# Optimization experiments

Measured on AMD Instinct MI355X. Metric: run time of the kernel, lower is better.

## Reference

```python
import jax, jax.numpy as jnp
import numpy as np

N_NODES = 100000

def _sage_conv(x, src, dst, Wl, bl, Wr, n_nodes):
    # PyG SAGEConv (mean aggr): out = lin_l(mean_{j in N(i)} x_j) + lin_r(x_i)
    msgs = x[src]                                            # [E, d] gather
    agg = jax.ops.segment_sum(msgs, dst, num_segments=n_nodes)   # [N, d]
    cnt = jax.ops.segment_sum(jnp.ones((src.shape[0],), x.dtype), dst,
                              num_segments=n_nodes)          # [N]
    mean = agg / jnp.maximum(cnt, 1.0)[:, None]              # mean aggregation
    return mean @ Wl.T + bl + x @ Wr.T

def setup_inputs() -> dict:
    key = jax.random.key(0)
    ks = jax.random.split(key, 6)
    d_in, d_hid, d_out = 64, 64, 2
    n_edges = 1600000
    x = jax.random.normal(ks[0], (N_NODES, d_in), dtype=jnp.float32)
    edge_index = jax.random.randint(ks[1], (2, n_edges), 0, N_NODES, dtype=jnp.int64)
    s = 1.0 / np.sqrt(d_in)
    W1l = jax.random.uniform(ks[2], (d_hid, d_in), jnp.float32, -s, s)
    b1l = jnp.zeros((d_hid,), jnp.float32)
    W1r = jax.random.uniform(ks[3], (d_hid, d_in), jnp.float32, -s, s)
    s2 = 1.0 / np.sqrt(d_hid)
    W2l = jax.random.uniform(ks[4], (d_out, d_hid), jnp.float32, -s2, s2)
    b2l = jnp.zeros((d_out,), jnp.float32)
    W2r = jax.random.uniform(ks[5], (d_out, d_hid), jnp.float32, -s2, s2)
    return {"x": x, "edge_index": edge_index, "W1l": W1l, "b1l": b1l,
            "W1r": W1r, "W2l": W2l, "b2l": b2l, "W2r": W2r}

def reference(x, edge_index, W1l, b1l, W1r, W2l, b2l, W2r):
    src, dst = edge_index[0], edge_index[1]
    h = _sage_conv(x, src, dst, W1l, b1l, W1r, N_NODES)
    h = jax.nn.relu(h)
    # F.dropout(p=0.5, training=False) is identity at inference
    out = _sage_conv(h, src, dst, W2l, b2l, W2r, N_NODES)
    return out
```

## Files before the change

kernel.cpp:

```cpp
#include <hip/hip_runtime.h>
#include <cstdint>

typedef long long i64;
typedef unsigned int u32;


#define BKT_SHIFT 8
#define BKT_MAX   512
#define BKT_CAP   5120
#define CHUNK     2048

__device__ __forceinline__ int edge_at(const void* eidx, int is64, size_t i) {
  return is64 ? (int)((const i64*)eidx)[i] : ((const int*)eidx)[i];
}

__global__ __launch_bounds__(256) void k_pre(const void* __restrict__ eidx,
                                             int* __restrict__ gcount, u32* __restrict__ pairs, int E,
                                             const float* __restrict__ x,
                                             const float* __restrict__ Wl, const float* __restrict__ bl,
                                             const float* __restrict__ Wr,
                                             float* __restrict__ XL, float* __restrict__ XR,
                                             int n_nodes, int nbkt) {
  __shared__ float smem[64 * 68 * 3];
  int tid = threadIdx.x;

  if ((int)blockIdx.x < nbkt) {
    int* hist   = (int*)smem;
    int* basech = hist + BKT_MAX;
    int* run    = basech + BKT_MAX;
    int* nzp    = run + BKT_MAX;
    for (int i = tid; i < BKT_MAX; i += 256) { hist[i] = 0; run[i] = 0; }
    if (tid == 0) *nzp = 0;
    __syncthreads();
    if (((const int*)eidx)[2 * tid + 1] != 0) *nzp = 1;
    __syncthreads();
    int is64 = (*nzp == 0);

    int cbase = blockIdx.x * CHUNK;
    int sreg[8], dreg[8];
#pragma unroll
    for (int i = 0; i < 8; ++i) {
      int e = cbase + tid + 256 * i;
      bool v = e < E;
      sreg[i] = v ? edge_at(eidx, is64, (size_t)e) : 0;
      dreg[i] = v ? edge_at(eidx, is64, (size_t)E + e) : -1;
      if (v) atomicAdd(&hist[dreg[i] >> BKT_SHIFT], 1);
    }
    __syncthreads();
    for (int i = tid; i < BKT_MAX; i += 256) {
      int h = hist[i];
      basech[i] = h ? (i * BKT_CAP + atomicAdd(&gcount[i], h)) : 0;
    }
    __syncthreads();
#pragma unroll
    for (int i = 0; i < 8; ++i) {
      if (dreg[i] >= 0) {
        int b = dreg[i] >> BKT_SHIFT;
        int r = atomicAdd(&run[b], 1);
        pairs[basech[b] + r] = ((u32)sreg[i] << 8) | (u32)(dreg[i] & 255);
      }
    }
    return;
  }

  float* sWl = smem;
  float* sWr = smem + 64 * 68;
  float* sX  = smem + 2 * 64 * 68;
  int base = (blockIdx.x - nbkt) * 64;

#pragma unroll
  for (int r = 0; r < 4; ++r) {
    int idx = tid + 256 * r;
    int f = idx >> 4, c4 = idx & 15;
    float4 wl = *(const float4*)(Wl + f * 64 + c4 * 4);
    float4 wr = *(const float4*)(Wr + f * 64 + c4 * 4);
    sWl[(c4 * 4 + 0) * 68 + f] = wl.x; sWl[(c4 * 4 + 1) * 68 + f] = wl.y;
    sWl[(c4 * 4 + 2) * 68 + f] = wl.z; sWl[(c4 * 4 + 3) * 68 + f] = wl.w;
    sWr[(c4 * 4 + 0) * 68 + f] = wr.x; sWr[(c4 * 4 + 1) * 68 + f] = wr.y;
    sWr[(c4 * 4 + 2) * 68 + f] = wr.z; sWr[(c4 * 4 + 3) * 68 + f] = wr.w;
  }
#pragma unroll
  for (int r = 0; r < 4; ++r) {
    int idx = tid + 256 * r;
    int nn = idx >> 4, c4 = idx & 15;
    int node = base + nn;
    float4 xv = make_float4(0.f, 0.f, 0.f, 0.f);
    if (node < n_nodes) xv = *(const float4*)(x + (size_t)node * 64 + c4 * 4);
    sX[(c4 * 4 + 0) * 68 + nn] = xv.x; sX[(c4 * 4 + 1) * 68 + nn] = xv.y;
    sX[(c4 * 4 + 2) * 68 + nn] = xv.z; sX[(c4 * 4 + 3) * 68 + nn] = xv.w;
  }
  __syncthreads();

  int f0 = (tid & 15) * 4, n0 = (tid >> 4) * 4;
  float accL[4][4] = {{0}}, accR[4][4] = {{0}};
#pragma unroll 8
  for (int k = 0; k < 64; ++k) {
    float4 xv = *(const float4*)&sX[k * 68 + n0];
    float4 wl = *(const float4*)&sWl[k * 68 + f0];
    float4 wr = *(const float4*)&sWr[k * 68 + f0];
    float xn[4] = {xv.x, xv.y, xv.z, xv.w};
    float wlf[4] = {wl.x, wl.y, wl.z, wl.w};
    float wrf[4] = {wr.x, wr.y, wr.z, wr.w};
#pragma unroll
    for (int a = 0; a < 4; ++a)
#pragma unroll
      for (int b = 0; b < 4; ++b) {
        accL[a][b] += xn[a] * wlf[b];
        accR[a][b] += xn[a] * wrf[b];
      }
  }

  float4 blv = *(const float4*)(bl + f0);
#pragma unroll
  for (int a = 0; a < 4; ++a) {
    int node = base + n0 + a;
    if (node >= n_nodes) continue;
    float4 ol = make_float4(accL[a][0], accL[a][1], accL[a][2], accL[a][3]);
    float4 orr = make_float4(accR[a][0] + blv.x, accR[a][1] + blv.y,
                             accR[a][2] + blv.z, accR[a][3] + blv.w);
    *(float4*)(XL + (size_t)node * 64 + f0) = ol;
    *(float4*)(XR + (size_t)node * 64 + f0) = orr;
  }
}

__global__ __launch_bounds__(512) void k_csr(const int* __restrict__ gcount, const u32* __restrict__ pairs,
                                             int* __restrict__ csr_src, int* __restrict__ rs,
                                             int* __restrict__ re, int n_nodes) {
  __shared__ int cnt[256];
  __shared__ int sc[256];
  __shared__ int cur[256];
  int b = blockIdx.x, t = threadIdx.x;
  if (t < 256) cnt[t] = 0;
  __syncthreads();
  int n = gcount[b];
  int lo = b * BKT_CAP, hi = lo + n;
  int tail = n & 3;
  for (int i = lo + t * 4; i + 3 < hi; i += 2048) {
    uint4 p = *(const uint4*)(pairs + i);
    atomicAdd(&cnt[p.x & 255], 1); atomicAdd(&cnt[p.y & 255], 1);
    atomicAdd(&cnt[p.z & 255], 1); atomicAdd(&cnt[p.w & 255], 1);
  }
  if (t < tail) atomicAdd(&cnt[pairs[hi - tail + t] & 255], 1);
  __syncthreads();
  int v = (t < 256) ? cnt[t] : 0;
  if (t < 256) sc[t] = v;
  __syncthreads();
  for (int off = 1; off < 256; off <<= 1) {
    int a = (t >= off && t < 256) ? sc[t - off] : 0;
    __syncthreads();
    if (t < 256) sc[t] += a;
    __syncthreads();
  }
  if (t < 256) {
    int start = lo + sc[t] - v;
    int node = (b << BKT_SHIFT) + t;
    if (node < n_nodes) { rs[node] = start; re[node] = start + v; }
    cur[t] = start;
  }
  __syncthreads();
  for (int i = lo + t * 4; i + 3 < hi; i += 2048) {
    uint4 p = *(const uint4*)(pairs + i);
    csr_src[atomicAdd(&cur[p.x & 255], 1)] = (int)(p.x >> 8);
    csr_src[atomicAdd(&cur[p.y & 255], 1)] = (int)(p.y >> 8);
    csr_src[atomicAdd(&cur[p.z & 255], 1)] = (int)(p.z >> 8);
    csr_src[atomicAdd(&cur[p.w & 255], 1)] = (int)(p.w >> 8);
  }
  if (t < tail) {
    u32 p = pairs[hi - tail + t];
    csr_src[atomicAdd(&cur[p & 255], 1)] = (int)(p >> 8);
  }
}

__global__ __launch_bounds__(256) void k_agg1g2(const int* __restrict__ rs, const int* __restrict__ re,
                                                const int* __restrict__ csr_src,
                                                const float* __restrict__ XL, const float* __restrict__ XR,
                                                const float* __restrict__ W2l, const float* __restrict__ b2l,
                                                const float* __restrict__ W2r,
                                                float* __restrict__ HL, float* __restrict__ HR,
                                                int n_nodes) {
  int wave = threadIdx.x >> 6, lane = threadIdx.x & 63;
  int g = lane >> 4, c = lane & 15;
  int n = (blockIdx.x * 4 + wave) * 4 + g;
  if (n >= n_nodes) return;

  float4 wl0 = *(const float4*)(W2l + c * 4);
  float4 wl1 = *(const float4*)(W2l + 64 + c * 4);
  float4 wr0 = *(const float4*)(W2r + c * 4);
  float4 wr1 = *(const float4*)(W2r + 64 + c * 4);
  float4 xr = *(const float4*)(XR + (size_t)n * 64 + c * 4);

  int start = rs[n], end = re[n];
  float4 a0 = make_float4(0.f, 0.f, 0.f, 0.f);
  float4 a1 = make_float4(0.f, 0.f, 0.f, 0.f);
  float4 a2 = make_float4(0.f, 0.f, 0.f, 0.f);
  float4 a3 = make_float4(0.f, 0.f, 0.f, 0.f);
  int e = start;
  for (; e + 7 < end; e += 8) {
    int s0 = csr_src[e],     s1 = csr_src[e + 1], s2 = csr_src[e + 2], s3 = csr_src[e + 3];
    int s4 = csr_src[e + 4], s5 = csr_src[e + 5], s6 = csr_src[e + 6], s7 = csr_src[e + 7];
    float4 v0 = *(const float4*)(XL + (size_t)s0 * 64 + c * 4);
    float4 v1 = *(const float4*)(XL + (size_t)s1 * 64 + c * 4);
    float4 v2 = *(const float4*)(XL + (size_t)s2 * 64 + c * 4);
    float4 v3 = *(const float4*)(XL + (size_t)s3 * 64 + c * 4);
    float4 v4 = *(const float4*)(XL + (size_t)s4 * 64 + c * 4);
    float4 v5 = *(const float4*)(XL + (size_t)s5 * 64 + c * 4);
    float4 v6 = *(const float4*)(XL + (size_t)s6 * 64 + c * 4);
    float4 v7 = *(const float4*)(XL + (size_t)s7 * 64 + c * 4);
    a0.x += v0.x; a0.y += v0.y; a0.z += v0.z; a0.w += v0.w;
    a1.x += v1.x; a1.y += v1.y; a1.z += v1.z; a1.w += v1.w;
    a2.x += v2.x; a2.y += v2.y; a2.z += v2.z; a2.w += v2.w;
    a3.x += v3.x; a3.y += v3.y; a3.z += v3.z; a3.w += v3.w;
    a0.x += v4.x; a0.y += v4.y; a0.z += v4.z; a0.w += v4.w;
    a1.x += v5.x; a1.y += v5.y; a1.z += v5.z; a1.w += v5.w;
    a2.x += v6.x; a2.y += v6.y; a2.z += v6.z; a2.w += v6.w;
    a3.x += v7.x; a3.y += v7.y; a3.z += v7.z; a3.w += v7.w;
  }
  for (; e + 3 < end; e += 4) {
    int s0 = csr_src[e], s1 = csr_src[e + 1], s2 = csr_src[e + 2], s3 = csr_src[e + 3];
    float4 v0 = *(const float4*)(XL + (size_t)s0 * 64 + c * 4);
    float4 v1 = *(const float4*)(XL + (size_t)s1 * 64 + c * 4);
    float4 v2 = *(const float4*)(XL + (size_t)s2 * 64 + c * 4);
    float4 v3 = *(const float4*)(XL + (size_t)s3 * 64 + c * 4);
    a0.x += v0.x; a0.y += v0.y; a0.z += v0.z; a0.w += v0.w;
    a1.x += v1.x; a1.y += v1.y; a1.z += v1.z; a1.w += v1.w;
    a2.x += v2.x; a2.y += v2.y; a2.z += v2.z; a2.w += v2.w;
    a3.x += v3.x; a3.y += v3.y; a3.z += v3.z; a3.w += v3.w;
  }
  if (e + 1 < end) {
    int s0 = csr_src[e], s1 = csr_src[e + 1];
    float4 v0 = *(const float4*)(XL + (size_t)s0 * 64 + c * 4);
    float4 v1 = *(const float4*)(XL + (size_t)s1 * 64 + c * 4);
    a0.x += v0.x; a0.y += v0.y; a0.z += v0.z; a0.w += v0.w;
    a1.x += v1.x; a1.y += v1.y; a1.z += v1.z; a1.w += v1.w;
    e += 2;
  }
  if (e < end) {
    int s0 = csr_src[e];
    float4 v0 = *(const float4*)(XL + (size_t)s0 * 64 + c * 4);
    a0.x += v0.x; a0.y += v0.y; a0.z += v0.z; a0.w += v0.w;
  }
  float inv = 1.0f / fmaxf((float)(end - start), 1.0f);
  float4 h;
  h.x = fmaxf((a0.x + a1.x + a2.x + a3.x) * inv + xr.x, 0.f);
  h.y = fmaxf((a0.y + a1.y + a2.y + a3.y) * inv + xr.y, 0.f);
  h.z = fmaxf((a0.z + a1.z + a2.z + a3.z) * inv + xr.z, 0.f);
  h.w = fmaxf((a0.w + a1.w + a2.w + a3.w) * inv + xr.w, 0.f);

  float p0 = h.x * wl0.x + h.y * wl0.y + h.z * wl0.z + h.w * wl0.w;
  float p1 = h.x * wl1.x + h.y * wl1.y + h.z * wl1.z + h.w * wl1.w;
  float q0 = h.x * wr0.x + h.y * wr0.y + h.z * wr0.z + h.w * wr0.w;
  float q1 = h.x * wr1.x + h.y * wr1.y + h.z * wr1.z + h.w * wr1.w;
#pragma unroll
  for (int off = 1; off < 16; off <<= 1) {
    p0 += __shfl_xor(p0, off, 16);
    p1 += __shfl_xor(p1, off, 16);
    q0 += __shfl_xor(q0, off, 16);
    q1 += __shfl_xor(q1, off, 16);
  }
  if (c == 0) {
    *(float2*)(HL + (size_t)n * 2) = make_float2(p0, p1);
    *(float2*)(HR + (size_t)n * 2) = make_float2(q0 + b2l[0], q1 + b2l[1]);
  }
}

__global__ __launch_bounds__(256) void k_agg2(const int* __restrict__ rs, const int* __restrict__ re,
                                              const int* __restrict__ csr_src,
                                              const float* __restrict__ HL, const float* __restrict__ HR,
                                              float* __restrict__ out, int n_nodes) {
  int n = blockIdx.x * 256 + threadIdx.x;
  if (n >= n_nodes) return;
  int start = rs[n], end = re[n];
  float s0 = 0.f, s1 = 0.f;
  int e = start;
  for (; e + 1 < end; e += 2) {
    int sa = csr_src[e], sb = csr_src[e + 1];
    float2 va = *(const float2*)(HL + (size_t)sa * 2);
    float2 vb = *(const float2*)(HL + (size_t)sb * 2);
    s0 += va.x + vb.x; s1 += va.y + vb.y;
  }
  if (e < end) {
    int sa = csr_src[e];
    float2 va = *(const float2*)(HL + (size_t)sa * 2);
    s0 += va.x; s1 += va.y;
  }
  float inv = 1.0f / fmaxf((float)(end - start), 1.0f);
  float2 hr = *(const float2*)(HR + (size_t)n * 2);
  out[n * 2 + 0] = s0 * inv + hr.x;
  out[n * 2 + 1] = s1 * inv + hr.y;
}

extern "C" void kernel_launch(void* const* d_in, const int* in_sizes, int n_in,
                              void* d_out, int out_size, void* d_ws, size_t ws_size,
                              hipStream_t stream) {
  const float* x   = (const float*)d_in[0];
  const void*  eix = d_in[1];
  const float* W1l = (const float*)d_in[2];
  const float* b1l = (const float*)d_in[3];
  const float* W1r = (const float*)d_in[4];
  const float* W2l = (const float*)d_in[5];
  const float* b2l = (const float*)d_in[6];
  const float* W2r = (const float*)d_in[7];
  float* out = (float*)d_out;

  const int N = in_sizes[0] / 64;
  const int E = in_sizes[1] / 2;
  const int NB = (N + 255) >> BKT_SHIFT;

  char* base = (char*)d_ws;
  size_t off = 0;
  auto alloc = [&](size_t bytes) {
    char* p = base + off;
    off = (off + bytes + 255) & ~(size_t)255;
    return p;
  };
  int*   gcount  = (int*)alloc((size_t)BKT_MAX * 4);
  int*   rs      = (int*)alloc((size_t)N * 4);
  int*   re      = (int*)alloc((size_t)N * 4);
  int*   csr_src = (int*)alloc((size_t)NB * BKT_CAP * 4);
  u32*   pairs   = (u32*)alloc((size_t)NB * BKT_CAP * 4);
  float* XL      = (float*)alloc((size_t)N * 64 * 4);
  float* XR      = (float*)alloc((size_t)N * 64 * 4);
  float* HL      = (float*)alloc((size_t)N * 2 * 4);
  float* HR      = (float*)alloc((size_t)N * 2 * 4);
  (void)ws_size;

  const int nbkt = (E + CHUNK - 1) / CHUNK;
  const int ngem = (N + 63) / 64;

  hipMemsetAsync(gcount, 0, (size_t)BKT_MAX * 4, stream);
  k_pre<<<nbkt + ngem, 256, 0, stream>>>(eix, gcount, pairs, E,
                                         x, W1l, b1l, W1r, XL, XR, N, nbkt);
  k_csr<<<NB, 512, 0, stream>>>(gcount, pairs, csr_src, rs, re, N);
  k_agg1g2<<<(N + 15) / 16, 256, 0, stream>>>(rs, re, csr_src, XL, XR, W2l, b2l, W2r, HL, HR, N);
  k_agg2<<<(N + 255) / 256, 256, 0, stream>>>(rs, re, csr_src, HL, HR, out, N);
}
```

Measured before the change: 219.4 us.

## Stage bucketed edge pairs in shared memory and interleave bucket and GEMM blocks

Each bucketing block now handles twice as many edges (sixteen per thread). It builds a local prefix scan over bucket counts, sorts its packed edge pairs by bucket in shared memory, and then writes them out in a grouped pass rather than scattering each edge straight to global memory. Bucketing blocks are also interleaved one in five with the XL/XR GEMM blocks, so the two kinds of work run side by side instead of in separate block ranges. The aim is more contiguous global writes and better overlap, at the cost of extra syncs and shared memory. The grid size now assumes four GEMM blocks per bucket block are enough to cover all nodes, which holds for these input sizes.

```diff
diff --git a/kernel.cpp b/kernel.cpp
--- a/kernel.cpp
+++ b/kernel.cpp
@@ -8,7 +8,8 @@
 #define BKT_SHIFT 8
 #define BKT_MAX   512
 #define BKT_CAP   5120
-#define CHUNK     2048
+#define CHUNK     4096
+#define EPT       16
 
 __device__ __forceinline__ int edge_at(const void* eidx, int is64, size_t i) {
   return is64 ? (int)((const i64*)eidx)[i] : ((const int*)eidx)[i];
@@ -20,15 +21,20 @@
                                              const float* __restrict__ Wl, const float* __restrict__ bl,
                                              const float* __restrict__ Wr,
                                              float* __restrict__ XL, float* __restrict__ XR,
-                                             int n_nodes, int nbkt) {
+                                             int n_nodes, int nbkt, int ngem) {
   __shared__ float smem[64 * 68 * 3];
   int tid = threadIdx.x;
-
-  if ((int)blockIdx.x < nbkt) {
-    int* hist   = (int*)smem;
-    int* basech = hist + BKT_MAX;
-    int* run    = basech + BKT_MAX;
-    int* nzp    = run + BKT_MAX;
+  int bid = blockIdx.x;
+
+  if (bid % 5 == 0) {
+    int b5 = bid / 5;
+    int* hist  = (int*)smem;
+    int* lbase = hist + BKT_MAX;
+    int* gbase = lbase + BKT_MAX;
+    int* run   = gbase + BKT_MAX;
+    int* nzp   = run + BKT_MAX;
+    u32* sg    = (u32*)(nzp + 1);
+    u32* sv    = sg + CHUNK;
     for (int i = tid; i < BKT_MAX; i += 256) { hist[i] = 0; run[i] = 0; }
     if (tid == 0) *nzp = 0;
     __syncthreads();
@@ -36,10 +42,10 @@
     __syncthreads();
     int is64 = (*nzp == 0);
 
-    int cbase = blockIdx.x * CHUNK;
-    int sreg[8], dreg[8];
-#pragma unroll
-    for (int i = 0; i < 8; ++i) {
+    int cbase = b5 * CHUNK;
+    int sreg[EPT], dreg[EPT];
+#pragma unroll
+    for (int i = 0; i < EPT; ++i) {
       int e = cbase + tid + 256 * i;
       bool v = e < E;
       sreg[i] = v ? edge_at(eidx, is64, (size_t)e) : 0;
@@ -47,26 +53,46 @@
       if (v) atomicAdd(&hist[dreg[i] >> BKT_SHIFT], 1);
     }
     __syncthreads();
-    for (int i = tid; i < BKT_MAX; i += 256) {
-      int h = hist[i];
-      basech[i] = h ? (i * BKT_CAP + atomicAdd(&gcount[i], h)) : 0;
+    int h0 = hist[2 * tid], h1 = hist[2 * tid + 1];
+    int ps = h0 + h1;
+    int* sc = (int*)sv;
+    sc[tid] = ps;
+    __syncthreads();
+    for (int off = 1; off < 256; off <<= 1) {
+      int a = (tid >= off) ? sc[tid - off] : 0;
+      __syncthreads();
+      sc[tid] += a;
+      __syncthreads();
     }
-    __syncthreads();
-#pragma unroll
-    for (int i = 0; i < 8; ++i) {
+    int excl = sc[tid] - ps;
+    lbase[2 * tid]     = excl;
+    lbase[2 * tid + 1] = excl + h0;
+    gbase[2 * tid]     = h0 ? (2 * tid) * BKT_CAP + atomicAdd(&gcount[2 * tid], h0) : 0;
+    gbase[2 * tid + 1] = h1 ? (2 * tid + 1) * BKT_CAP + atomicAdd(&gcount[2 * tid + 1], h1) : 0;
+    __syncthreads();
+#pragma unroll
+    for (int i = 0; i < EPT; ++i) {
       if (dreg[i] >= 0) {
         int b = dreg[i] >> BKT_SHIFT;
         int r = atomicAdd(&run[b], 1);
-        pairs[basech[b] + r] = ((u32)sreg[i] << 8) | (u32)(dreg[i] & 255);
+        int p = lbase[b] + r;
+        sg[p] = gbase[b] + r;
+        sv[p] = ((u32)sreg[i] << 8) | (u32)(dreg[i] & 255);
       }
     }
+    __syncthreads();
+    int total = min(E - cbase, CHUNK);
+    for (int i = tid; i < total; i += 256)
+      pairs[sg[i]] = sv[i];
     return;
   }
 
+  int g = bid - bid / 5 - 1;
+  if (g >= ngem) return;
   float* sWl = smem;
   float* sWr = smem + 64 * 68;
   float* sX  = smem + 2 * 64 * 68;
-  int base = (blockIdx.x - nbkt) * 64;
+  int base = g * 64;
 
 #pragma unroll
   for (int r = 0; r < 4; ++r) {
@@ -328,8 +354,8 @@
   const int ngem = (N + 63) / 64;
 
   hipMemsetAsync(gcount, 0, (size_t)BKT_MAX * 4, stream);
-  k_pre<<<nbkt + ngem, 256, 0, stream>>>(eix, gcount, pairs, E,
-                                         x, W1l, b1l, W1r, XL, XR, N, nbkt);
+  k_pre<<<5 * nbkt, 256, 0, stream>>>(eix, gcount, pairs, E,
+                                      x, W1l, b1l, W1r, XL, XR, N, nbkt, ngem);
   k_csr<<<NB, 512, 0, stream>>>(gcount, pairs, csr_src, rs, re, N);
   k_agg1g2<<<(N + 15) / 16, 256, 0, stream>>>(rs, re, csr_src, XL, XR, W2l, b2l, W2r, HL, HR, N);
   k_agg2<<<(N + 255) / 256, 256, 0, stream>>>(rs, re, csr_src, HL, HR, out, N);
```

Result: faster. 202.2 us (-7.8%).
